# Kernel optimization log

Measured on AMD Instinct MI355X. Metric: run time of the kernel, lower is better.

Reference implementation:

```python
import jax, jax.numpy as jnp
import numpy as np

ALPHA = 0.5
BETA = 5.0
LOGIT_SCALE = 100.0  # exp(log(100)) -- CLIP's learned logit scale at its clamp value
NUM_CLASSES = 200


def _l2norm(x):
    return x / jnp.linalg.norm(x, axis=-1, keepdims=True)


def setup_inputs() -> dict:
    key = jax.random.key(0)
    k1, k2, k3, k4 = jax.random.split(key, 4)
    img_f = jax.random.normal(k1, (1024, 512), dtype=jnp.float32)
    text_features = jax.random.normal(k2, (200, 512), dtype=jnp.float32)
    keys = jax.random.normal(k3, (50000, 512), dtype=jnp.float32)
    labels = jax.random.randint(k4, (50000,), 0, NUM_CLASSES, dtype=jnp.int64)
    return {"img_f": img_f, "text_features": text_features, "keys": keys, "labels": labels}


def reference(img_f, text_features, keys, labels):
    # encode_image output is L2-normalized in the module; keys were built from
    # normalized image features, text_features are normalized class embeddings.
    q = _l2norm(img_f)            # [B, D]
    t = _l2norm(text_features)    # [C, D]
    k = _l2norm(keys)             # [N, D]

    # CLIP zero-shot branch: scale * q @ t.T -> [B, C]
    z = LOGIT_SCALE * jnp.einsum('bd,cd->bc', q, t)

    # Tip-Adapter cache branch: exp(beta * q @ keys.T) @ one_hot(labels)
    sim = jnp.einsum('bd,nd->bn', q, k)                 # [B, N]
    aff = jnp.exp(BETA * sim)                           # [B, N]
    values = jax.nn.one_hot(labels, NUM_CLASSES, dtype=aff.dtype)  # [N, C]
    c = aff @ values                                    # [B, C]

    return (1.0 - ALPHA) * z + ALPHA * c
```

## Files before the change

### kernel.cpp

```cpp
#include <hip/hip_runtime.h>

#define B_Q    1024
#define D_K    512
#define N_CLS  200
#define N_KEYS 50000
#define N_PAD  50048
#define N_ZT   (N_PAD / 128)
#define NT_TOT (N_ZT + 2)
#define KN_ROWS 50304
#define HS     16

#define R0 N_PAD
#define R1 (R0 + B_Q)
#define R2 (R1 + N_CLS)
#define R3 (R2 + 56)
#define R4 (R3 + 400)

typedef __attribute__((ext_vector_type(8))) short bf16x8;
typedef __attribute__((ext_vector_type(4))) float f32x4;

__device__ __forceinline__ unsigned short f2bf(float f) {
  union { float f; unsigned int i; } v; v.f = f;
  unsigned int r = v.i + 0x7fffu + ((v.i >> 16) & 1u);
  return (unsigned short)(r >> 16);
}
__device__ __forceinline__ uint4 pack8(const float f[8], float s) {
  uint4 o;
  o.x = (unsigned)f2bf(f[0]*s) | ((unsigned)f2bf(f[1]*s) << 16);
  o.y = (unsigned)f2bf(f[2]*s) | ((unsigned)f2bf(f[3]*s) << 16);
  o.z = (unsigned)f2bf(f[4]*s) | ((unsigned)f2bf(f[5]*s) << 16);
  o.w = (unsigned)f2bf(f[6]*s) | ((unsigned)f2bf(f[7]*s) << 16);
  return o;
}
__device__ __forceinline__ void async_copy16(const void* g, void* lds) {
  __builtin_amdgcn_global_load_lds(
      (const __attribute__((address_space(1))) unsigned int*)g,
      (__attribute__((address_space(3))) unsigned int*)lds, 16, 0, 0);
}

__global__ void k_zero(int* __restrict__ g) {
  int i = blockIdx.x * 1024 + threadIdx.x;
  if (i < 2 * N_CLS * HS) g[i] = 0;
}

__global__ __launch_bounds__(1024) void k_rank(const int* __restrict__ labels,
                                               const int* __restrict__ ghist,
                                               int* __restrict__ gcnt,
                                               int* __restrict__ perm,
                                               int* __restrict__ cls) {
  __shared__ int incl[N_CLS];
  __shared__ int histl[N_CLS];
  __shared__ int lhist[N_CLS];
  __shared__ int lbase[N_CLS];
  __shared__ int lcur[N_CLS];
  int t = threadIdx.x;
  if (t < N_CLS) {
    int h = ghist[t * HS];
    histl[t] = h; incl[t] = h; lhist[t] = 0;
  }
  __syncthreads();
  for (int d = 1; d < N_CLS; d <<= 1) {
    int x = 0;
    if (t < N_CLS && t >= d) x = incl[t - d];
    __syncthreads();
    if (t < N_CLS) incl[t] += x;
    __syncthreads();
  }
  int n = blockIdx.x * 1024 + t;
  int lab = -1;
  if (n < N_KEYS) {
    lab = labels[n];
    atomicAdd(&lhist[lab], 1);
  }
  __syncthreads();
  if (t < N_CLS && lhist[t] > 0) {
    lbase[t] = (incl[t] - histl[t]) + atomicAdd(&gcnt[t * HS], lhist[t]);
    lcur[t] = 0;
  }
  __syncthreads();
  if (n < N_KEYS) {
    int r = atomicAdd(&lcur[lab], 1);
    int d = lbase[lab] + r;
    perm[d] = n;
    cls[d] = lab;
  } else if (n < KN_ROWS) {
    perm[n] = n;
    cls[n] = N_CLS;
  }
}

__global__ void k_prep2(const float* __restrict__ keys, const float* __restrict__ img,
                        const float* __restrict__ txt, const int* __restrict__ labels,
                        unsigned short* __restrict__ qn, unsigned short* __restrict__ kn,
                        int* __restrict__ ghist, float* __restrict__ out) {
  int w = threadIdx.x >> 6, lane = threadIdx.x & 63;
  int row = blockIdx.x * 4 + w;
  const float* src; unsigned short* dst;
  if (row < R0) {
    if (row >= N_KEYS) {
      *((uint4*)(kn + (size_t)row * D_K) + lane) = make_uint4(0, 0, 0, 0);
      return;
    }
    if (lane == 0) atomicAdd(&ghist[labels[row] * HS], 1);
    src = keys + (size_t)row * D_K;
    dst = kn + (size_t)row * D_K;
  } else if (row < R1) {
    int r = row - R0;
    src = img + (size_t)r * D_K;
    dst = qn + (size_t)r * D_K;
  } else if (row < R2) {
    int r = row - R1;
    src = txt + (size_t)r * D_K;
    dst = kn + (size_t)(N_PAD + r) * D_K;
  } else if (row < R3) {
    int r = N_PAD + N_CLS + (row - R2);
    *((uint4*)(kn + (size_t)r * D_K) + lane) = make_uint4(0, 0, 0, 0);
    return;
  } else if (row < R4) {
    int zr = row - R3;
    uint4* o4 = (uint4*)(out + (size_t)zr * 512) + lane * 2;
    o4[0] = make_uint4(0, 0, 0, 0);
    o4[1] = make_uint4(0, 0, 0, 0);
    return;
  } else return;
  const float4* s4 = (const float4*)src + lane * 2;
  float4 a = s4[0], b = s4[1];
  float f[8] = {a.x, a.y, a.z, a.w, b.x, b.y, b.z, b.w};
  float ss = 0.f;
#pragma unroll
  for (int i = 0; i < 8; i++) ss += f[i] * f[i];
#pragma unroll
  for (int d = 1; d < 64; d <<= 1) ss += __shfl_xor(ss, d);
  float rinv = rsqrtf(ss);
  *((uint4*)dst + lane) = pack8(f, rinv);
}

__global__ __launch_bounds__(256, 3) void k_main(const unsigned short* __restrict__ qn,
                                                 const unsigned short* __restrict__ kn,
                                                 const int* __restrict__ cls,
                                                 const int* __restrict__ perm,
                                                 float* __restrict__ out) {
  __shared__ unsigned short As[128 * 64];
  __shared__ unsigned short Bs[128 * 64];
  int t = threadIdx.x;
  int wsw = (blockIdx.x & 7) * NT_TOT + (blockIdx.x >> 3);
  int tileN = wsw >> 3, tileB = wsw & 7;
  int rowB0 = tileB * 128, rowN0 = tileN * 128;

  f32x4 acc[4][4];
#pragma unroll
  for (int i = 0; i < 4; i++)
#pragma unroll
    for (int j = 0; j < 4; j++) acc[i][j] = (f32x4){0.f, 0.f, 0.f, 0.f};

  int lane = t & 63, w = t >> 6;
  int wr = (w >> 1) * 64, wc = (w & 1) * 64;
  int l15 = lane & 15, lq = lane >> 4;
  const int rA = t >> 3;
  const int gsw = ((t & 7) ^ (rA & 7)) * 8;
  const int sw = l15 & 7;

  int prow[4];
#pragma unroll
  for (int i = 0; i < 4; i++) prow[i] = perm[rowN0 + i * 32 + rA];
  int cj[4];
#pragma unroll
  for (int j = 0; j < 4; j++) cj[j] = cls[rowN0 + wc + 16 * j + l15];
  int cseg0 = cls[rowN0 + wc];
  int cseg1 = cls[rowN0 + wc + 63];

  for (int k0 = 0; k0 < D_K; k0 += 64) {
    __syncthreads();
#pragma unroll
    for (int i = 0; i < 4; i++) {
      int row = i * 32 + rA;
      async_copy16(qn + (size_t)(rowB0 + row) * D_K + k0 + gsw, &As[i * 2048 + t * 8]);
      async_copy16(kn + (size_t)prow[i] * D_K + k0 + gsw, &Bs[i * 2048 + t * 8]);
    }
    __syncthreads();
#pragma unroll
    for (int ks = 0; ks < 64; ks += 32) {
      bf16x8 af[4], bf[4];
#pragma unroll
      for (int i = 0; i < 4; i++)
        af[i] = *(const bf16x8*)&As[(wr + 16 * i + l15) * 64 + ((((ks >> 3) + lq) ^ sw) * 8)];
#pragma unroll
      for (int j = 0; j < 4; j++)
        bf[j] = *(const bf16x8*)&Bs[(wc + 16 * j + l15) * 64 + ((((ks >> 3) + lq) ^ sw) * 8)];
#pragma unroll
      for (int i = 0; i < 4; i++)
#pragma unroll
        for (int j = 0; j < 4; j++)
          acc[i][j] = __builtin_amdgcn_mfma_f32_16x16x32_bf16(af[i], bf[j], acc[i][j], 0, 0, 0);
    }
  }

  if (tileN >= N_ZT) {
#pragma unroll
    for (int i = 0; i < 4; i++)
#pragma unroll
      for (int j = 0; j < 4; j++) {
        int col = rowN0 + wc + 16 * j + l15 - N_PAD;
        if (col < N_CLS) {
#pragma unroll
          for (int r = 0; r < 4; r++) {
            int row = rowB0 + wr + 16 * i + lq * 4 + r;
            atomicAdd(out + (size_t)row * N_CLS + col, 50.0f * acc[i][j][r]);
          }
        }
      }
    return;
  }

#pragma unroll
  for (int i = 0; i < 4; i++)
#pragma unroll
    for (int j = 0; j < 4; j++)
#pragma unroll
      for (int r = 0; r < 4; r++) acc[i][j][r] = __expf(5.0f * acc[i][j][r]);

  for (int c = cseg0; c <= cseg1; c++) {
    if (c >= N_CLS) break;
#pragma unroll
    for (int i = 0; i < 4; i++) {
      float s0 = 0.f, s1 = 0.f, s2 = 0.f, s3 = 0.f;
#pragma unroll
      for (int j = 0; j < 4; j++) {
        if (cj[j] == c) {
          s0 += acc[i][j][0]; s1 += acc[i][j][1];
          s2 += acc[i][j][2]; s3 += acc[i][j][3];
        }
      }
#pragma unroll
      for (int d = 1; d < 16; d <<= 1) {
        s0 += __shfl_xor(s0, d); s1 += __shfl_xor(s1, d);
        s2 += __shfl_xor(s2, d); s3 += __shfl_xor(s3, d);
      }
      if (l15 == 0) {
        int row = rowB0 + wr + 16 * i + lq * 4;
        float* o = out + (size_t)row * N_CLS + c;
        if (s0 != 0.f) atomicAdd(o + 0 * N_CLS, 0.5f * s0);
        if (s1 != 0.f) atomicAdd(o + 1 * N_CLS, 0.5f * s1);
        if (s2 != 0.f) atomicAdd(o + 2 * N_CLS, 0.5f * s2);
        if (s3 != 0.f) atomicAdd(o + 3 * N_CLS, 0.5f * s3);
      }
    }
  }
}

extern "C" void kernel_launch(void* const* d_in, const int* in_sizes, int n_in,
                              void* d_out, int out_size, void* d_ws, size_t ws_size,
                              hipStream_t stream) {
  (void)in_sizes; (void)n_in; (void)out_size; (void)ws_size;
  const float* img    = (const float*)d_in[0];
  const float* txt    = (const float*)d_in[1];
  const float* keys   = (const float*)d_in[2];
  const int*   labels = (const int*)d_in[3];
  float*       out    = (float*)d_out;

  char* ws = (char*)d_ws;
  unsigned short* qn = (unsigned short*)(ws + 0);
  unsigned short* kn = (unsigned short*)(ws + 1048576);
  int*  perm = (int*)(ws + 52559872);
  int*  cls  = (int*)(ws + 52761088);
  int*  gz   = (int*)(ws + 52962304);

  k_zero<<<7, 1024, 0, stream>>>(gz);
  k_prep2<<<(R4 + 3) / 4, 256, 0, stream>>>(keys, img, txt, labels, qn, kn, gz, out);
  k_rank<<<(KN_ROWS + 1023) / 1024, 1024, 0, stream>>>(labels, gz, gz + N_CLS * HS, perm, cls);
  k_main<<<dim3(8 * NT_TOT), 256, 0, stream>>>(qn, kn, cls, perm, out);
}
```

Measured before the change: 252.1 us.

## Enlarge GEMM tiles to 256x256 with double-buffered LDS pipeline

The main kernel moves from 128x128 tiles with 256 threads to 256x256 tiles with 512 threads, each wave holding an 8x4 accumulator set. It stages A and B into double-buffered dynamic shared memory (128KB) and interleaves the next-stage async copies with MFMA quads, raising wave priority around the MFMA work. Padding rows of the key matrix now point at a single text row instead of being zero-filled, which removes prep work and lets perm/cls cover exactly the padded range. The changes aim to improve data reuse per load and overlap memory with compute. The costs are higher register pressure and lower occupancy, plus fewer, larger blocks that may balance less evenly across CUs.

```diff
diff --git a/kernel.cpp b/kernel.cpp
--- a/kernel.cpp
+++ b/kernel.cpp
@@ -4,17 +4,16 @@
 #define D_K    512
 #define N_CLS  200
 #define N_KEYS 50000
-#define N_PAD  50048
-#define N_ZT   (N_PAD / 128)
-#define NT_TOT (N_ZT + 2)
-#define KN_ROWS 50304
+#define N_PAD  50176
+#define N_ZT   196
+#define NT_TOT 197
+#define KN_ROWS 50200
 #define HS     16
 
-#define R0 N_PAD
-#define R1 (R0 + B_Q)
-#define R2 (R1 + N_CLS)
-#define R3 (R2 + 56)
-#define R4 (R3 + 400)
+#define PR0 N_KEYS
+#define PR1 (PR0 + B_Q)
+#define PR2 (PR1 + N_CLS)
+#define PR3 (PR2 + 400)
 
 typedef __attribute__((ext_vector_type(8))) short bf16x8;
 typedef __attribute__((ext_vector_type(4))) float f32x4;
@@ -83,8 +82,8 @@
     int d = lbase[lab] + r;
     perm[d] = n;
     cls[d] = lab;
-  } else if (n < KN_ROWS) {
-    perm[n] = n;
+  } else if (n < N_PAD) {
+    perm[n] = N_KEYS;
     cls[n] = N_CLS;
   }
 }
@@ -96,28 +95,20 @@
   int w = threadIdx.x >> 6, lane = threadIdx.x & 63;
   int row = blockIdx.x * 4 + w;
   const float* src; unsigned short* dst;
-  if (row < R0) {
-    if (row >= N_KEYS) {
-      *((uint4*)(kn + (size_t)row * D_K) + lane) = make_uint4(0, 0, 0, 0);
-      return;
-    }
+  if (row < PR0) {
     if (lane == 0) atomicAdd(&ghist[labels[row] * HS], 1);
     src = keys + (size_t)row * D_K;
     dst = kn + (size_t)row * D_K;
-  } else if (row < R1) {
-    int r = row - R0;
+  } else if (row < PR1) {
+    int r = row - PR0;
     src = img + (size_t)r * D_K;
     dst = qn + (size_t)r * D_K;
-  } else if (row < R2) {
-    int r = row - R1;
+  } else if (row < PR2) {
+    int r = row - PR1;
     src = txt + (size_t)r * D_K;
-    dst = kn + (size_t)(N_PAD + r) * D_K;
-  } else if (row < R3) {
-    int r = N_PAD + N_CLS + (row - R2);
-    *((uint4*)(kn + (size_t)r * D_K) + lane) = make_uint4(0, 0, 0, 0);
-    return;
-  } else if (row < R4) {
-    int zr = row - R3;
+    dst = kn + (size_t)(N_KEYS + r) * D_K;
+  } else if (row < PR3) {
+    int zr = row - PR2;
     uint4* o4 = (uint4*)(out + (size_t)zr * 512) + lane * 2;
     o4[0] = make_uint4(0, 0, 0, 0);
     o4[1] = make_uint4(0, 0, 0, 0);
@@ -135,76 +126,119 @@
   *((uint4*)dst + lane) = pack8(f, rinv);
 }
 
-__global__ __launch_bounds__(256, 3) void k_main(const unsigned short* __restrict__ qn,
+__global__ __launch_bounds__(512, 2) void k_main(const unsigned short* __restrict__ qn,
                                                  const unsigned short* __restrict__ kn,
                                                  const int* __restrict__ cls,
                                                  const int* __restrict__ perm,
                                                  float* __restrict__ out) {
-  __shared__ unsigned short As[128 * 64];
-  __shared__ unsigned short Bs[128 * 64];
+  extern __shared__ unsigned short smem[];
   int t = threadIdx.x;
-  int wsw = (blockIdx.x & 7) * NT_TOT + (blockIdx.x >> 3);
-  int tileN = wsw >> 3, tileB = wsw & 7;
-  int rowB0 = tileB * 128, rowN0 = tileN * 128;
-
-  f32x4 acc[4][4];
-#pragma unroll
-  for (int i = 0; i < 4; i++)
+  int bid = blockIdx.x;
+  int xcd = bid & 7, bk = bid >> 3;
+  int wsw = (xcd < 4 ? xcd * 99 : 396 + (xcd - 4) * 98) + bk;
+  int tileN = wsw >> 2, tileB = wsw & 3;
+  int rowB0 = tileB * 256, rowN0 = tileN * 256;
+
+  f32x4 acc[8][4];
+#pragma unroll
+  for (int i = 0; i < 8; i++)
 #pragma unroll
     for (int j = 0; j < 4; j++) acc[i][j] = (f32x4){0.f, 0.f, 0.f, 0.f};
 
   int lane = t & 63, w = t >> 6;
-  int wr = (w >> 1) * 64, wc = (w & 1) * 64;
+  int wm = (w >> 2) * 128;
+  int wcN = (w & 3) * 64;
   int l15 = lane & 15, lq = lane >> 4;
   const int rA = t >> 3;
   const int gsw = ((t & 7) ^ (rA & 7)) * 8;
   const int sw = l15 & 7;
 
   int prow[4];
-#pragma unroll
-  for (int i = 0; i < 4; i++) prow[i] = perm[rowN0 + i * 32 + rA];
-  int cj[4];
-#pragma unroll
-  for (int j = 0; j < 4; j++) cj[j] = cls[rowN0 + wc + 16 * j + l15];
-  int cseg0 = cls[rowN0 + wc];
-  int cseg1 = cls[rowN0 + wc + 63];
-
-  for (int k0 = 0; k0 < D_K; k0 += 64) {
+  int cj[4] = {N_CLS, N_CLS, N_CLS, N_CLS};
+  int cseg0 = N_CLS, cseg1 = N_CLS;
+  if (tileN < N_ZT) {
+#pragma unroll
+    for (int c = 0; c < 4; c++) prow[c] = perm[rowN0 + c * 64 + rA];
+#pragma unroll
+    for (int j = 0; j < 4; j++) cj[j] = cls[rowN0 + wcN + 16 * j + l15];
+    cseg0 = cls[rowN0 + wcN];
+    cseg1 = cls[rowN0 + wcN + 63];
+  } else {
+#pragma unroll
+    for (int c = 0; c < 4; c++) {
+      int r = c * 64 + rA;
+      prow[c] = N_KEYS + (r < N_CLS ? r : N_CLS - 1);
+    }
+  }
+
+  auto stageA = [&](int p, int k0) {
+    unsigned short* dst = smem + p * 16384;
+#pragma unroll
+    for (int c = 0; c < 4; c++)
+      async_copy16(qn + (size_t)(rowB0 + c * 64 + rA) * D_K + k0 + gsw,
+                   dst + c * 4096 + t * 8);
+  };
+  auto stageB = [&](int p, int k0) {
+    unsigned short* dst = smem + 32768 + p * 16384;
+#pragma unroll
+    for (int c = 0; c < 4; c++)
+      async_copy16(kn + (size_t)prow[c] * D_K + k0 + gsw,
+                   dst + c * 4096 + t * 8);
+  };
+  auto quad = [&](int p, int ih, int jh) {
+    const unsigned short* A = smem + p * 16384;
+    const unsigned short* B = smem + 32768 + p * 16384;
+    __builtin_amdgcn_s_setprio(1);
+#pragma unroll
+    for (int s = 0; s < 2; s++) {
+      int cg = ((s * 4 + lq) ^ sw) * 8;
+      bf16x8 af[4], bf[2];
+#pragma unroll
+      for (int i = 0; i < 4; i++) {
+        int ra = wm + ih * 64 + 16 * i + l15;
+        af[i] = *(const bf16x8*)&A[ra * 64 + cg];
+      }
+#pragma unroll
+      for (int jj = 0; jj < 2; jj++) {
+        int rb = wcN + (jh * 2 + jj) * 16 + l15;
+        bf[jj] = *(const bf16x8*)&B[rb * 64 + cg];
+      }
+#pragma unroll
+      for (int i = 0; i < 4; i++)
+#pragma unroll
+        for (int jj = 0; jj < 2; jj++)
+          acc[ih * 4 + i][jh * 2 + jj] = __builtin_amdgcn_mfma_f32_16x16x32_bf16(
+              af[i], bf[jj], acc[ih * 4 + i][jh * 2 + jj], 0, 0, 0);
+    }
+    __builtin_amdgcn_s_setprio(0);
+  };
+
+  stageA(0, 0); stageB(0, 0);
+  __syncthreads();
+  for (int kt = 0; kt < 8; ++kt) {
+    int p = kt & 1, k0n = (kt + 1) * 64;
+    if (kt < 7) stageA(p ^ 1, k0n);
+    quad(p, 0, 0);
+    __builtin_amdgcn_s_barrier();
+    if (kt < 7) stageB(p ^ 1, k0n);
+    quad(p, 0, 1);
+    __builtin_amdgcn_s_barrier();
+    quad(p, 1, 0);
+    __builtin_amdgcn_s_barrier();
+    quad(p, 1, 1);
     __syncthreads();
-#pragma unroll
-    for (int i = 0; i < 4; i++) {
-      int row = i * 32 + rA;
-      async_copy16(qn + (size_t)(rowB0 + row) * D_K + k0 + gsw, &As[i * 2048 + t * 8]);
-      async_copy16(kn + (size_t)prow[i] * D_K + k0 + gsw, &Bs[i * 2048 + t * 8]);
-    }
-    __syncthreads();
-#pragma unroll
-    for (int ks = 0; ks < 64; ks += 32) {
-      bf16x8 af[4], bf[4];
-#pragma unroll
-      for (int i = 0; i < 4; i++)
-        af[i] = *(const bf16x8*)&As[(wr + 16 * i + l15) * 64 + ((((ks >> 3) + lq) ^ sw) * 8)];
-#pragma unroll
-      for (int j = 0; j < 4; j++)
-        bf[j] = *(const bf16x8*)&Bs[(wc + 16 * j + l15) * 64 + ((((ks >> 3) + lq) ^ sw) * 8)];
-#pragma unroll
-      for (int i = 0; i < 4; i++)
-#pragma unroll
-        for (int j = 0; j < 4; j++)
-          acc[i][j] = __builtin_amdgcn_mfma_f32_16x16x32_bf16(af[i], bf[j], acc[i][j], 0, 0, 0);
-    }
   }
 
   if (tileN >= N_ZT) {
 #pragma unroll
-    for (int i = 0; i < 4; i++)
+    for (int i = 0; i < 8; i++)
 #pragma unroll
       for (int j = 0; j < 4; j++) {
-        int col = rowN0 + wc + 16 * j + l15 - N_PAD;
+        int col = wcN + 16 * j + l15;
         if (col < N_CLS) {
 #pragma unroll
           for (int r = 0; r < 4; r++) {
-            int row = rowB0 + wr + 16 * i + lq * 4 + r;
+            int row = rowB0 + wm + 16 * i + lq * 4 + r;
             atomicAdd(out + (size_t)row * N_CLS + col, 50.0f * acc[i][j][r]);
           }
         }
@@ -213,7 +247,7 @@
   }
 
 #pragma unroll
-  for (int i = 0; i < 4; i++)
+  for (int i = 0; i < 8; i++)
 #pragma unroll
     for (int j = 0; j < 4; j++)
 #pragma unroll
@@ -222,7 +256,7 @@
   for (int c = cseg0; c <= cseg1; c++) {
     if (c >= N_CLS) break;
 #pragma unroll
-    for (int i = 0; i < 4; i++) {
+    for (int i = 0; i < 8; i++) {
       float s0 = 0.f, s1 = 0.f, s2 = 0.f, s3 = 0.f;
 #pragma unroll
       for (int j = 0; j < 4; j++) {
@@ -237,7 +271,7 @@
         s2 += __shfl_xor(s2, d); s3 += __shfl_xor(s3, d);
       }
       if (l15 == 0) {
-        int row = rowB0 + wr + 16 * i + lq * 4;
+        int row = rowB0 + wm + 16 * i + lq * 4;
         float* o = out + (size_t)row * N_CLS + c;
         if (s0 != 0.f) atomicAdd(o + 0 * N_CLS, 0.5f * s0);
         if (s1 != 0.f) atomicAdd(o + 1 * N_CLS, 0.5f * s1);
@@ -261,12 +295,15 @@
   char* ws = (char*)d_ws;
   unsigned short* qn = (unsigned short*)(ws + 0);
   unsigned short* kn = (unsigned short*)(ws + 1048576);
-  int*  perm = (int*)(ws + 52559872);
-  int*  cls  = (int*)(ws + 52761088);
-  int*  gz   = (int*)(ws + 52962304);
+  int*  perm = (int*)(ws + 52453376);
+  int*  cls  = (int*)(ws + 52654080);
+  int*  gz   = (int*)(ws + 52854784);
+
+  hipFuncSetAttribute((const void*)k_main,
+                      hipFuncAttributeMaxDynamicSharedMemorySize, 131072);
 
   k_zero<<<7, 1024, 0, stream>>>(gz);
-  k_prep2<<<(R4 + 3) / 4, 256, 0, stream>>>(keys, img, txt, labels, qn, kn, gz, out);
-  k_rank<<<(KN_ROWS + 1023) / 1024, 1024, 0, stream>>>(labels, gz, gz + N_CLS * HS, perm, cls);
-  k_main<<<dim3(8 * NT_TOT), 256, 0, stream>>>(qn, kn, cls, perm, out);
-}
+  k_prep2<<<(PR3 + 3) / 4, 256, 0, stream>>>(keys, img, txt, labels, qn, kn, gz, out);
+  k_rank<<<N_PAD / 1024, 1024, 0, stream>>>(labels, gz, gz + N_CLS * HS, perm, cls);
+  k_main<<<dim3(4 * NT_TOT), 512, 131072, stream>>>(qn, kn, cls, perm, out);
+}
```

New measurement: 290.1 us. 15.1% more time.
